# Optimization experiments

Hardware: AMD Instinct MI355X
Metric: run time of the kernel (lower is better)

Reference implementation:

```python
import jax, jax.numpy as jnp
import numpy as np

NEG = -65504.0  # torch.finfo(float16).min
EPS = 1e-6

B, T, D = 2, 1024, 2048
H, HD = 16, 128          # n_head, head_dim
K = 128                  # dynamic_w_hidden_dim
IH = 1                   # dynamic_hidden_dim = H // squeeze_ratio


def _rope(x, freqs_cis):
    # x: [B,T,H,hd]; 'half' mode: first/second half are the rotation pair,
    # output is interleaved (stack(...,-1).flatten(3) in torch).
    half = x.shape[-1] // 2
    a, b = x[..., :half], x[..., half:]
    cos = freqs_cis[None, :, None, :, 0]
    sin = freqs_cis[None, :, None, :, 1]
    out = jnp.stack([a * cos - b * sin, b * cos + a * sin], axis=-1)
    return out.reshape(x.shape)


def _cross_head_proj(inputs, qw1, qw2, kw1, kw2, qdd, kdd):
    # inputs: [B,N,T,S]; qw1/qw2: [B,T,I,N]; kw1/kw2: [B,S,I,N]; qdd: [B,T,N]; kdd: [B,S,N]
    out = inputs
    out = out + jnp.einsum('bnts,btin,btim->bmts', inputs, qw1, qw2)
    out = out + jnp.einsum('bnts,bsin,bsim->bmts', inputs, kw1, kw2)
    out = out + inputs * jnp.swapaxes(qdd, 1, 2)[..., None]   # [B,N,T,1]
    out = out + inputs * jnp.swapaxes(kdd, 1, 2)[:, :, None, :]  # [B,N,1,S]
    return out


def setup_inputs() -> dict:
    key = jax.random.key(0)
    ks = jax.random.split(key, 7)
    x = jax.random.normal(ks[0], (B, T, D), jnp.float32)
    mask = jnp.tril(jnp.ones((1, 1, T, T), bool))  # causal
    # rotary tables: [T, hd/2, 2] (cos, sin)
    inv = 1.0 / (10000.0 ** (jnp.arange(0, HD, 2, dtype=jnp.float32) / HD))
    ang = jnp.arange(T, dtype=jnp.float32)[:, None] * inv[None, :]
    freqs_cis = jnp.stack([jnp.cos(ang), jnp.sin(ang)], axis=-1)
    s = 0.02
    wqkv = jax.random.normal(ks[1], (D, 3 * H * HD), jnp.float32) * s
    wo = jax.random.normal(ks[2], (H * HD, D), jnp.float32) * s
    dw1 = jax.random.normal(ks[3], (D, 4, K), jnp.float32) * s
    qkw = jax.random.normal(ks[4], (4, K, 2 * IH, H), jnp.float32) * s
    dd_w = jax.random.normal(ks[5], (D, 4 * H), jnp.float32) * s
    return {"x": x, "mask": mask, "freqs_cis": freqs_cis, "wqkv": wqkv,
            "wo": wo, "dw1": dw1, "qkw": qkw, "dd_w": dd_w}


def reference(x, mask, freqs_cis, wqkv, wo, dw1, qkw, dd_w):
    b, t, d = x.shape
    qkv = x @ wqkv
    q, k, v = jnp.split(qkv, [H * HD, 2 * H * HD], axis=-1)
    q = q.reshape(b, t, H, HD)
    k = k.reshape(b, t, H, HD)
    v = v.reshape(b, t, H, HD)
    q = _rope(q, freqs_cis)
    k = _rope(k, freqs_cis)
    q = jnp.swapaxes(q, 1, 2) * (HD ** -0.5)  # [B,H,T,hd]
    k = jnp.swapaxes(k, 1, 2)
    v = jnp.swapaxes(v, 1, 2)

    # ---- DynamicWeightProjection (G=1, squeezed) ----
    dw_hidden = jax.nn.gelu(jnp.einsum('btd,dck->btck', x, dw1), approximate=False)
    w = jnp.einsum('btck,ckim->btcim', dw_hidden, qkw)  # [B,T,4,2*IH,H]
    w1, w2 = w[..., :IH, :], w[..., IH:, :]
    w1 = w1 * jax.lax.rsqrt(jnp.mean(w1 * w1, axis=-1, keepdims=True) + EPS)
    pre_qw1, pre_kw1, post_qw1, post_kw1 = [w1[:, :, i] for i in range(4)]
    pre_qw2, pre_kw2, post_qw2, post_kw2 = [w2[:, :, i] for i in range(4)]
    dd = jnp.tanh(x @ dd_w).reshape(b, t, 4, H)
    pre_qdd, pre_kdd, post_qdd, post_kdd = [dd[:, :, i] for i in range(4)]

    # ---- attention with cross-head mixing ----
    logits = jnp.einsum('bhtd,bhsd->bhts', q, k)
    logits = _cross_head_proj(logits, pre_qw1, pre_qw2, pre_kw1, pre_kw2, pre_qdd, pre_kdd)
    logits = jnp.where(mask, logits, NEG)
    probs = jax.nn.softmax(logits, axis=-1)
    probs = _cross_head_proj(probs, post_qw1, post_qw2, post_kw1, post_kw2, post_qdd, post_kdd)
    o = jnp.einsum('bhts,bhsd->bhtd', probs, v)
    o = jnp.swapaxes(o, 1, 2).reshape(b, t, H * HD)
    return o @ wo
```

## Files before the change

kernel.cpp:

```cpp
#include <hip/hip_runtime.h>


typedef unsigned short u16;
typedef unsigned int u32;
typedef __attribute__((ext_vector_type(8))) short s16x8;
typedef __attribute__((ext_vector_type(4))) float f32x4;
typedef __attribute__((ext_vector_type(2))) float f32x2;
typedef __attribute__((ext_vector_type(2))) u16 u16x2;
typedef __attribute__((ext_vector_type(8))) u16 u16x8;

#define DEV __device__ __forceinline__

DEV float bf2f(u16 u) { union { u32 u; float f; } a; a.u = ((u32)u) << 16; return a.f; }
DEV u16 f2bf(float f) {
  union { float f; u32 u; } a; a.f = f;
  u32 r = a.u + 0x7fffu + ((a.u >> 16) & 1u);
  return (u16)(r >> 16);
}

DEV void gload16(const void* g, void* l) {
  __builtin_amdgcn_global_load_lds((__attribute__((address_space(1))) void*)g,
                                   (__attribute__((address_space(3))) void*)l,
                                   16, 0, 0);
}

template <int OUTBF>
__global__ __launch_bounds__(256) void gemm_bt(
    const u16* __restrict__ A, const u16* __restrict__ B, void* __restrict__ Cp,
    int K, int lda, int ldb, int ldc,
    long sAb, long sBb, long sCb1, long sCb2, int CZ2, int cmode, int swz)
{
  int bx = blockIdx.x, by = blockIdx.y;
  if (swz) {
    int nx = gridDim.x;
    int fid = by * nx + bx;
    int cpx = (nx * gridDim.y) >> 3;
    int nid = (fid & 7) * cpx + (fid >> 3);
    bx = nid % nx; by = nid / nx;
  }
  if (cmode == 1 && bx > by) return;
  __shared__ u16 sA[128 * 64];
  __shared__ u16 sB[128 * 64];
  const int tid = threadIdx.x, wv = tid >> 6, ln = tid & 63;
  const int z = blockIdx.z;
  const u16* Ab = A + (size_t)z * sAb + (size_t)(by * 128) * lda;
  const u16* Bb = B + (size_t)z * sBb + (size_t)(bx * 128) * ldb;
  const int wr = (wv >> 1) * 64, wc = (wv & 1) * 64;
  const int Keff = (cmode == 2) ? min(K, (by + 1) * 128) : K;

  f32x4 acc[4][4];
#pragma unroll
  for (int m = 0; m < 4; ++m)
#pragma unroll
    for (int n = 0; n < 4; ++n) {
      f32x4 zz = {0.f, 0.f, 0.f, 0.f};
      acc[m][n] = zz;
    }

  int o_[4], r_[4], cb_[4];
#pragma unroll
  for (int i = 0; i < 4; ++i) {
    int o = (wv * 4 + i) * 1024 + ln * 16;
    o_[i] = o;
    int r = o >> 7;
    r_[i] = r;
    cb_[i] = (o & 127) ^ ((r & 7) << 4);
  }
  const int frswz = (ln & 7) << 4;
  const int fkcol = (ln >> 4) << 4;

  for (int k0 = 0; k0 < Keff; k0 += 64) {
    __syncthreads();
#pragma unroll
    for (int i = 0; i < 4; ++i)
      gload16(Ab + (size_t)r_[i] * lda + (k0 + (cb_[i] >> 1)), (char*)sA + o_[i]);
#pragma unroll
    for (int i = 0; i < 4; ++i)
      gload16(Bb + (size_t)r_[i] * ldb + (k0 + (cb_[i] >> 1)), (char*)sB + o_[i]);
    __syncthreads();

#pragma unroll
    for (int ks = 0; ks < 2; ++ks) {
      s16x8 av[4], bv[4];
#pragma unroll
      for (int m = 0; m < 4; ++m) {
        int row = wr + m * 16 + (ln & 15);
        int addr = row * 128 + ((ks * 64 + fkcol) ^ frswz);
        av[m] = *(const s16x8*)((const char*)sA + addr);
      }
#pragma unroll
      for (int n = 0; n < 4; ++n) {
        int row = wc + n * 16 + (ln & 15);
        int addr = row * 128 + ((ks * 64 + fkcol) ^ frswz);
        bv[n] = *(const s16x8*)((const char*)sB + addr);
      }
#pragma unroll
      for (int m = 0; m < 4; ++m)
#pragma unroll
        for (int n = 0; n < 4; ++n)
          acc[m][n] = __builtin_amdgcn_mfma_f32_16x16x32_bf16(av[m], bv[n], acc[m][n], 0, 0, 0);
    }
  }

  const size_t cbase = (size_t)(z / CZ2) * sCb1 + (size_t)(z % CZ2) * sCb2;
  const int r0 = by * 128 + wr + ((ln >> 4) << 2);
  const int c0 = bx * 128 + wc + (ln & 15);
#pragma unroll
  for (int m = 0; m < 4; ++m)
#pragma unroll
    for (int n = 0; n < 4; ++n)
#pragma unroll
      for (int j = 0; j < 4; ++j) {
        int row = r0 + m * 16 + j, col = c0 + n * 16;
        if (OUTBF)
          ((u16*)Cp)[cbase + (size_t)row * ldc + col] = f2bf(acc[m][n][j]);
        else
          ((float*)Cp)[cbase + (size_t)row * ldc + col] = acc[m][n][j];
      }
}

template <int INBF>
__global__ __launch_bounds__(256) void transpose_to_bf16(
    const void* __restrict__ srcv, u16* __restrict__ dst,
    int R, int C, int Cpad, int srcLd, long sSrc1, long sSrc2, int Z2, long sDst)
{
  __shared__ float tile[32][33];
  const int z = blockIdx.z, z1 = z / Z2, z2 = z % Z2;
  const size_t sbase = (size_t)z1 * sSrc1 + (size_t)z2 * sSrc2;
  u16* d = dst + (size_t)z * sDst;
  const int c0 = blockIdx.x * 32, r0 = blockIdx.y * 32;
  const int tx = threadIdx.x, ty = threadIdx.y;
#pragma unroll
  for (int i = 0; i < 4; ++i) {
    int r = r0 + ty + i * 8, c = c0 + tx;
    float v = 0.f;
    if (c < C && r < R) {
      if (INBF) v = bf2f(((const u16*)srcv)[sbase + (size_t)r * srcLd + c]);
      else      v = ((const float*)srcv)[sbase + (size_t)r * srcLd + c];
    }
    tile[ty + i * 8][tx] = v;
  }
  __syncthreads();
#pragma unroll
  for (int i = 0; i < 4; ++i) {
    int dr = c0 + ty + i * 8, dc = r0 + tx;
    if (dr < Cpad && dc < R) d[(size_t)dr * R + dc] = f2bf(tile[tx][ty + i * 8]);
  }
}

__global__ void cvt_f32_bf16_k(const float* __restrict__ src, u16* __restrict__ dst, int n4) {
  int i = blockIdx.x * 256 + threadIdx.x;
  if (i >= n4) return;
  const float4 v = ((const float4*)src)[i];
  u16* o = dst + (size_t)i * 4;
  o[0] = f2bf(v.x); o[1] = f2bf(v.y); o[2] = f2bf(v.z); o[3] = f2bf(v.w);
}

__global__ __launch_bounds__(256) void rope_k(
    const u16* __restrict__ qkvm, const float* __restrict__ fc,
    u16* __restrict__ qb, u16* __restrict__ kb)
{
  const int bt = blockIdx.x, b = bt >> 10, t = bt & 1023;
  const u16* row = qkvm + (size_t)bt * 6784;
  const float SC = 0.08838834764831845f;
#pragma unroll
  for (int it = 0; it < 4; ++it) {
    int idx = threadIdx.x + it * 256;
    int h = idx >> 6, j = idx & 63;
    float c = fc[(t * 64 + j) * 2], sn = fc[(t * 64 + j) * 2 + 1];
    float qa = bf2f(row[h * 128 + j]), qbv = bf2f(row[h * 128 + 64 + j]);
    float ka = bf2f(row[2048 + h * 128 + j]), kbv = bf2f(row[2048 + h * 128 + 64 + j]);
    size_t o = ((size_t)(b * 16 + h) * 1024 + t) * 128 + 2 * j;
    qb[o]     = f2bf((qa * c - qbv * sn) * SC);
    qb[o + 1] = f2bf((qbv * c + qa * sn) * SC);
    kb[o]     = f2bf(ka * c - kbv * sn);
    kb[o + 1] = f2bf(kbv * c + ka * sn);
  }
}

__global__ __launch_bounds__(64) void gelu_bf16_k(u16* __restrict__ qm) {
  int bt = blockIdx.x, tid = threadIdx.x;
  u16* p = qm + (size_t)bt * 6784 + 6144 + tid * 8;
  u16x8 v = *(u16x8*)p;
#pragma unroll
  for (int i = 0; i < 8; ++i) {
    float f = bf2f(v[i]);
    f = 0.5f * f * (1.f + erff(f * 0.70710678118654752f));
    v[i] = f2bf(f);
  }
  *(u16x8*)p = v;
}

__global__ __launch_bounds__(64) void wproj_k(
    const u16* __restrict__ qkvm, const float* __restrict__ qkw,
    float* __restrict__ w1a, float* __restrict__ w2a, float* __restrict__ kpT)
{
  const int bt = blockIdx.x, ln = threadIdx.x;
  const int c = ln >> 4, m = ln & 15;
  const int b = bt >> 10, t = bt & 1023;
  const u16* hp = qkvm + (size_t)bt * 6784 + 6144 + c * 128;
  const float* Wp = qkw + (size_t)c * 4096 + m;
  float w1 = 0.f, w2 = 0.f;
  for (int k = 0; k < 128; ++k) {
    float hv = bf2f(hp[k]);
    w1 += hv * Wp[k * 32];
    w2 += hv * Wp[k * 32 + 16];
  }
  float ss = w1 * w1;
  ss += __shfl_xor(ss, 1); ss += __shfl_xor(ss, 2);
  ss += __shfl_xor(ss, 4); ss += __shfl_xor(ss, 8);
  float nrm = rsqrtf(ss * (1.f / 16.f) + 1e-6f);
  float w1n = w1 * nrm;
  size_t o = (size_t)bt * 64 + c * 16 + m;
  w1a[o] = w1n;
  w2a[o] = w2;
  size_t kb = (size_t)b * 98304 + (size_t)m * 1024 + t;
  if (c == 1) { kpT[kb] = w1n; kpT[kb + 16384] = w2; }
  if (c == 3) { kpT[kb + 49152] = w1n; kpT[kb + 65536] = w2; }
}

__global__ __launch_bounds__(64) void dd_k(const u16* __restrict__ qkvm,
                                           float* __restrict__ dda, float* __restrict__ kpT) {
  int bt = blockIdx.x, ln = threadIdx.x;
  int c = ln >> 4, m = ln & 15;
  int b = bt >> 10, t = bt & 1023;
  float v = tanhf(bf2f(qkvm[(size_t)bt * 6784 + 6656 + ln]));
  dda[(size_t)bt * 64 + ln] = v;
  size_t kb = (size_t)b * 98304 + (size_t)m * 1024 + t;
  if (c == 1) kpT[kb + 32768] = v;
  if (c == 3) kpT[kb + 81920] = v;
}

__global__ __launch_bounds__(512, 2) void proj_softmax_k(
    const float* __restrict__ L, u16* __restrict__ P,
    const float* __restrict__ w1a, const float* __restrict__ w2a,
    const float* __restrict__ dda, const float* __restrict__ kparT)
{
  const int t0 = blockIdx.x * 2, b = blockIdx.y;
  const int tid = threadIdx.x, wv = tid >> 6, ln = tid & 63;
  const int s0 = tid * 2;
  const bool liveB = (s0 <= t0 + 1);

  __shared__ float qpar[2][6][16];
  __shared__ float red2[2][16][8];
  __shared__ float rzf[2][16];
  if (tid < 192) {
    int tt = (tid >= 96) ? 1 : 0, u = tid - tt * 96;
    int a = u >> 4, hh = u & 15;
    const float* sp = (a == 0 || a == 3) ? w1a : ((a == 1 || a == 4) ? w2a : dda);
    int cc = (a < 3) ? 0 : 2;
    qpar[tt][a][hh] = sp[(size_t)(b * 1024 + t0 + tt) * 64 + cc * 16 + hh];
  }
  __syncthreads();

  const float* kp = kparT + (size_t)b * 98304 + s0;
  float vA[16][2], vB[16][2];
  const size_t lbaseA = ((size_t)(b * 16) * 1024 + t0) * 1024 + s0;
  const size_t lbaseB = lbaseA + 1024;

  if (liveB) {
#pragma unroll
    for (int h = 0; h < 16; ++h) {
      f32x2 dA = *(const f32x2*)(L + lbaseA + (size_t)h * 1048576);
      f32x2 dB = *(const f32x2*)(L + lbaseB + (size_t)h * 1048576);
      vA[h][0] = dA[0]; vA[h][1] = dA[1];
      vB[h][0] = dB[0]; vB[h][1] = dB[1];
    }
    float dqA0 = 0.f, dqA1 = 0.f, dkA0 = 0.f, dkA1 = 0.f;
    float dqB0 = 0.f, dqB1 = 0.f, dkB0 = 0.f, dkB1 = 0.f;
#pragma unroll
    for (int h = 0; h < 16; ++h) {
      f32x2 k1 = *(const f32x2*)(kp + h * 1024);
      dqA0 += vA[h][0] * qpar[0][0][h]; dqA1 += vA[h][1] * qpar[0][0][h];
      dkA0 += vA[h][0] * k1[0];         dkA1 += vA[h][1] * k1[1];
      dqB0 += vB[h][0] * qpar[1][0][h]; dqB1 += vB[h][1] * qpar[1][0][h];
      dkB0 += vB[h][0] * k1[0];         dkB1 += vB[h][1] * k1[1];
    }
    const bool okA0 = (s0 <= t0), okA1 = (s0 + 1 <= t0), okB1 = (s0 + 1 <= t0 + 1);
#pragma unroll
    for (int h = 0; h < 16; ++h) {
      f32x2 k2 = *(const f32x2*)(kp + 16384 + h * 1024);
      f32x2 kd = *(const f32x2*)(kp + 32768 + h * 1024);
      float aA0 = vA[h][0] * (1.f + qpar[0][2][h] + kd[0]) + qpar[0][1][h] * dqA0 + k2[0] * dkA0;
      float aA1 = vA[h][1] * (1.f + qpar[0][2][h] + kd[1]) + qpar[0][1][h] * dqA1 + k2[1] * dkA1;
      float aB0 = vB[h][0] * (1.f + qpar[1][2][h] + kd[0]) + qpar[1][1][h] * dqB0 + k2[0] * dkB0;
      float aB1 = vB[h][1] * (1.f + qpar[1][2][h] + kd[1]) + qpar[1][1][h] * dqB1 + k2[1] * dkB1;
      vA[h][0] = okA0 ? __expf(aA0) : 0.f;
      vA[h][1] = okA1 ? __expf(aA1) : 0.f;
      vB[h][0] = __expf(aB0);
      vB[h][1] = okB1 ? __expf(aB1) : 0.f;
    }
  } else {
#pragma unroll
    for (int h = 0; h < 16; ++h) {
      vA[h][0] = 0.f; vA[h][1] = 0.f; vB[h][0] = 0.f; vB[h][1] = 0.f;
    }
  }

#pragma unroll
  for (int h = 0; h < 16; ++h) {
    float xA = vA[h][0] + vA[h][1];
    float xB = vB[h][0] + vB[h][1];
#pragma unroll
    for (int off = 32; off > 0; off >>= 1) {
      xA += __shfl_xor(xA, off);
      xB += __shfl_xor(xB, off);
    }
    if (ln == 0) { red2[0][h][wv] = xA; red2[1][h][wv] = xB; }
  }
  __syncthreads();
  if (tid < 32) {
    int tt = tid >> 4, h = tid & 15;
    rzf[tt][h] = 1.f / (((red2[tt][h][0] + red2[tt][h][1]) + (red2[tt][h][2] + red2[tt][h][3])) +
                        ((red2[tt][h][4] + red2[tt][h][5]) + (red2[tt][h][6] + red2[tt][h][7])));
  }
  __syncthreads();

  const size_t pbaseA = lbaseA, pbaseB = lbaseB;
  if (liveB) {
    float pdqA0 = 0.f, pdqA1 = 0.f, pdkA0 = 0.f, pdkA1 = 0.f;
    float pdqB0 = 0.f, pdqB1 = 0.f, pdkB0 = 0.f, pdkB1 = 0.f;
#pragma unroll
    for (int h = 0; h < 16; ++h) {
      f32x2 k1 = *(const f32x2*)(kp + 49152 + h * 1024);
      float rzA = rzf[0][h], rzB = rzf[1][h];
      float pA0 = vA[h][0] * rzA, pA1 = vA[h][1] * rzA;
      float pB0 = vB[h][0] * rzB, pB1 = vB[h][1] * rzB;
      vA[h][0] = pA0; vA[h][1] = pA1; vB[h][0] = pB0; vB[h][1] = pB1;
      pdqA0 += pA0 * qpar[0][3][h]; pdqA1 += pA1 * qpar[0][3][h];
      pdkA0 += pA0 * k1[0];         pdkA1 += pA1 * k1[1];
      pdqB0 += pB0 * qpar[1][3][h]; pdqB1 += pB1 * qpar[1][3][h];
      pdkB0 += pB0 * k1[0];         pdkB1 += pB1 * k1[1];
    }
#pragma unroll
    for (int h = 0; h < 16; ++h) {
      f32x2 k2 = *(const f32x2*)(kp + 65536 + h * 1024);
      f32x2 kd = *(const f32x2*)(kp + 81920 + h * 1024);
      u16x2 pkA, pkB;
      pkA[0] = f2bf(vA[h][0] * (1.f + qpar[0][5][h] + kd[0]) + qpar[0][4][h] * pdqA0 + k2[0] * pdkA0);
      pkA[1] = f2bf(vA[h][1] * (1.f + qpar[0][5][h] + kd[1]) + qpar[0][4][h] * pdqA1 + k2[1] * pdkA1);
      pkB[0] = f2bf(vB[h][0] * (1.f + qpar[1][5][h] + kd[0]) + qpar[1][4][h] * pdqB0 + k2[0] * pdkB0);
      pkB[1] = f2bf(vB[h][1] * (1.f + qpar[1][5][h] + kd[1]) + qpar[1][4][h] * pdqB1 + k2[1] * pdkB1);
      *(u16x2*)(P + pbaseA + (size_t)h * 1048576) = pkA;
      *(u16x2*)(P + pbaseB + (size_t)h * 1048576) = pkB;
    }
  } else {
    u16x2 z2 = {0, 0};
#pragma unroll
    for (int h = 0; h < 16; ++h) {
      *(u16x2*)(P + pbaseA + (size_t)h * 1048576) = z2;
      *(u16x2*)(P + pbaseB + (size_t)h * 1048576) = z2;
    }
  }
}

extern "C" void kernel_launch(void* const* d_in, const int* in_sizes, int n_in,
                              void* d_out, int out_size, void* d_ws, size_t ws_size,
                              hipStream_t stream)
{
  (void)in_sizes; (void)n_in; (void)out_size; (void)ws_size;
  const float* x    = (const float*)d_in[0];
  const float* fc   = (const float*)d_in[2];
  const float* wqkv = (const float*)d_in[3];
  const float* wo   = (const float*)d_in[4];
  const float* dw1  = (const float*)d_in[5];
  const float* qkw  = (const float*)d_in[6];
  const float* ddw  = (const float*)d_in[7];
  float* out = (float*)d_out;
  char* w = (char*)d_ws;

  u16*   woT   = (u16*)(w + 0);
  u16*   qb    = (u16*)(w + 8388608);
  u16*   kb    = (u16*)(w + 16777216);
  u16*   vT    = (u16*)(w + 25165824);
  u16*   obf   = (u16*)(w + 33554432);
  float* w1a   = (float*)(w + 41943040);
  float* w2a   = (float*)(w + 42467328);
  float* dda   = (float*)(w + 42991616);
  const size_t TB = 43515904;
  u16*   xb    = (u16*)(w + TB);
  u16*   wallT = (u16*)(w + TB + 8388608);
  u16*   qkvm  = (u16*)(w + TB + 36175872);
  float* L     = (float*)(w + TB);
  u16*   P     = (u16*)(w + TB + 134217728);
  float* kparT = (float*)(w + 244842496);

  cvt_f32_bf16_k<<<4096, 256, 0, stream>>>(x, xb, 1048576);
  transpose_to_bf16<0><<<dim3(192, 64, 1), dim3(32, 8), 0, stream>>>(wqkv, wallT, 2048, 6144, 6144, 6144, 0, 0, 1, 0);
  transpose_to_bf16<0><<<dim3(16, 64, 1),  dim3(32, 8), 0, stream>>>(dw1,  wallT + (size_t)6144 * 2048, 2048, 512, 512, 512, 0, 0, 1, 0);
  transpose_to_bf16<0><<<dim3(4, 64, 1),   dim3(32, 8), 0, stream>>>(ddw,  wallT + (size_t)6656 * 2048, 2048, 64, 128, 64, 0, 0, 1, 0);
  transpose_to_bf16<0><<<dim3(64, 64, 1),  dim3(32, 8), 0, stream>>>(wo,   woT, 2048, 2048, 2048, 2048, 0, 0, 1, 0);

  gemm_bt<1><<<dim3(53, 16, 1), 256, 0, stream>>>(xb, wallT, qkvm, 2048, 2048, 2048, 6784, 0, 0, 0, 0, 1, 0, 1);
  rope_k<<<2048, 256, 0, stream>>>(qkvm, fc, qb, kb);
  transpose_to_bf16<1><<<dim3(4, 32, 32), dim3(32, 8), 0, stream>>>(qkvm + 4096, vT, 1024, 128, 128, 6784, 6946816, 128, 16, 131072);

  gelu_bf16_k<<<2048, 64, 0, stream>>>(qkvm);
  wproj_k<<<2048, 64, 0, stream>>>(qkvm, qkw, w1a, w2a, kparT);
  dd_k<<<2048, 64, 0, stream>>>(qkvm, dda, kparT);

  gemm_bt<0><<<dim3(8, 8, 32), 256, 0, stream>>>(qb, kb, L, 128, 128, 128, 1024, 131072, 131072, 1048576, 0, 1, 1, 0);
  proj_softmax_k<<<dim3(512, 2, 1), 512, 0, stream>>>(L, P, w1a, w2a, dda, kparT);
  gemm_bt<1><<<dim3(1, 8, 32), 256, 0, stream>>>(P, vT, obf, 1024, 1024, 1024, 2048, 1048576, 131072, 2097152, 128, 16, 2, 0);

  gemm_bt<0><<<dim3(16, 16, 1), 256, 0, stream>>>(obf, woT, out, 2048, 2048, 2048, 2048, 0, 0, 0, 0, 1, 0, 1);
}
```

Measured before the change: 325.1 us.

## Use 256x256 double-buffered MFMA GEMM for fused QKV/gating projection

```diff
diff --git a/kernel.cpp b/kernel.cpp
--- a/kernel.cpp
+++ b/kernel.cpp
@@ -22,6 +22,118 @@
   __builtin_amdgcn_global_load_lds((__attribute__((address_space(1))) void*)g,
                                    (__attribute__((address_space(3))) void*)l,
                                    16, 0, 0);
+}
+
+template <int OUTBF>
+__global__ __launch_bounds__(512, 1) void gemm256(
+    const u16* __restrict__ A, const u16* __restrict__ B, void* __restrict__ Cp,
+    int K, int lda, int ldb, int ldc)
+{
+  __shared__ u16 sA[2][256 * 64];
+  __shared__ u16 sB[2][256 * 64];
+  const int tid = threadIdx.x, ln = tid & 63;
+  const int wid = tid >> 6, wm = wid >> 2, wn = wid & 3;
+
+  const int nx = gridDim.x;
+  const int fid = blockIdx.y * nx + blockIdx.x;
+  const int cpx = (nx * gridDim.y) >> 3;
+  const int nid = (fid & 7) * cpx + (fid >> 3);
+  const int bx = nid % nx, by = nid / nx;
+
+  const u16* Ab = A + (size_t)(by * 256) * lda;
+  const u16* Bb = B + (size_t)(bx * 256) * ldb;
+
+  f32x4 acc[8][4];
+#pragma unroll
+  for (int m = 0; m < 8; ++m)
+#pragma unroll
+    for (int n = 0; n < 4; ++n) {
+      f32x4 zz = {0.f, 0.f, 0.f, 0.f};
+      acc[m][n] = zz;
+    }
+
+  int srow[4], scol[4], soff[4];
+#pragma unroll
+  for (int i = 0; i < 4; ++i) {
+    int o = i * 8192 + tid * 16;
+    soff[i] = o;
+    srow[i] = o >> 7;
+    scol[i] = (o & 127) >> 1;
+  }
+
+#define STAGE256(ba, bb, k0)                                              \
+  {                                                                       \
+    _Pragma("unroll")                                                     \
+    for (int i_ = 0; i_ < 4; ++i_)                                        \
+      gload16(Ab + (size_t)srow[i_] * lda + (k0) + scol[i_],              \
+              (char*)(ba) + soff[i_]);                                    \
+    _Pragma("unroll")                                                     \
+    for (int i_ = 0; i_ < 4; ++i_)                                        \
+      gload16(Bb + (size_t)srow[i_] * ldb + (k0) + scol[i_],              \
+              (char*)(bb) + soff[i_]);                                    \
+  }
+
+  const int arow = wm * 128 + (ln & 15);
+  const int brow = wn * 64 + (ln & 15);
+  const int kb = (ln >> 4) * 16;
+  const int NT = K >> 6;
+
+  STAGE256(sA[0], sB[0], 0);
+  asm volatile("s_waitcnt vmcnt(0)" ::: "memory");
+  __builtin_amdgcn_s_barrier();
+
+  for (int t = 0; t < NT; ++t) {
+    const int c = t & 1;
+    const char* pa = (const char*)sA[c];
+    const char* pb = (const char*)sB[c];
+    s16x8 bfr[4][2];
+#pragma unroll
+    for (int ph = 0; ph < 4; ++ph) {
+      if (ph == 0) {
+        if (t + 1 < NT) STAGE256(sA[c ^ 1], sB[c ^ 1], (t + 1) * 64);
+#pragma unroll
+        for (int n = 0; n < 4; ++n)
+#pragma unroll
+          for (int kk = 0; kk < 2; ++kk)
+            bfr[n][kk] = *(const s16x8*)(pb + (size_t)(brow + n * 16) * 128 + kk * 64 + kb);
+      }
+      s16x8 afr[2][2];
+#pragma unroll
+      for (int mm = 0; mm < 2; ++mm)
+#pragma unroll
+        for (int kk = 0; kk < 2; ++kk)
+          afr[mm][kk] = *(const s16x8*)(pa + (size_t)(arow + (ph * 2 + mm) * 16) * 128 + kk * 64 + kb);
+      __builtin_amdgcn_s_barrier();
+      __builtin_amdgcn_s_setprio(1);
+#pragma unroll
+      for (int mm = 0; mm < 2; ++mm)
+#pragma unroll
+        for (int n = 0; n < 4; ++n)
+#pragma unroll
+          for (int kk = 0; kk < 2; ++kk)
+            acc[ph * 2 + mm][n] = __builtin_amdgcn_mfma_f32_16x16x32_bf16(
+                afr[mm][kk], bfr[n][kk], acc[ph * 2 + mm][n], 0, 0, 0);
+      __builtin_amdgcn_s_setprio(0);
+    }
+    asm volatile("s_waitcnt vmcnt(0)" ::: "memory");
+    __builtin_amdgcn_s_barrier();
+  }
+#undef STAGE256
+
+  const int r0 = by * 256 + wm * 128 + ((ln >> 4) << 2);
+  const int c0 = bx * 256 + wn * 64 + (ln & 15);
+#pragma unroll
+  for (int m = 0; m < 8; ++m)
+#pragma unroll
+    for (int n = 0; n < 4; ++n)
+#pragma unroll
+      for (int j = 0; j < 4; ++j) {
+        int row = r0 + m * 16 + j, col = c0 + n * 16;
+        if (OUTBF)
+          ((u16*)Cp)[(size_t)row * ldc + col] = f2bf(acc[m][n][j]);
+        else
+          ((float*)Cp)[(size_t)row * ldc + col] = acc[m][n][j];
+      }
 }
 
 template <int OUTBF>
@@ -161,7 +273,7 @@
     u16* __restrict__ qb, u16* __restrict__ kb)
 {
   const int bt = blockIdx.x, b = bt >> 10, t = bt & 1023;
-  const u16* row = qkvm + (size_t)bt * 6784;
+  const u16* row = qkvm + (size_t)bt * 6912;
   const float SC = 0.08838834764831845f;
 #pragma unroll
   for (int it = 0; it < 4; ++it) {
@@ -180,7 +292,7 @@
 
 __global__ __launch_bounds__(64) void gelu_bf16_k(u16* __restrict__ qm) {
   int bt = blockIdx.x, tid = threadIdx.x;
-  u16* p = qm + (size_t)bt * 6784 + 6144 + tid * 8;
+  u16* p = qm + (size_t)bt * 6912 + 6144 + tid * 8;
   u16x8 v = *(u16x8*)p;
 #pragma unroll
   for (int i = 0; i < 8; ++i) {
@@ -198,7 +310,7 @@
   const int bt = blockIdx.x, ln = threadIdx.x;
   const int c = ln >> 4, m = ln & 15;
   const int b = bt >> 10, t = bt & 1023;
-  const u16* hp = qkvm + (size_t)bt * 6784 + 6144 + c * 128;
+  const u16* hp = qkvm + (size_t)bt * 6912 + 6144 + c * 128;
   const float* Wp = qkw + (size_t)c * 4096 + m;
   float w1 = 0.f, w2 = 0.f;
   for (int k = 0; k < 128; ++k) {
@@ -224,7 +336,7 @@
   int bt = blockIdx.x, ln = threadIdx.x;
   int c = ln >> 4, m = ln & 15;
   int b = bt >> 10, t = bt & 1023;
-  float v = tanhf(bf2f(qkvm[(size_t)bt * 6784 + 6656 + ln]));
+  float v = tanhf(bf2f(qkvm[(size_t)bt * 6912 + 6656 + ln]));
   dda[(size_t)bt * 64 + ln] = v;
   size_t kb = (size_t)b * 98304 + (size_t)m * 1024 + t;
   if (c == 1) kpT[kb + 32768] = v;
@@ -380,7 +492,7 @@
   const size_t TB = 43515904;
   u16*   xb    = (u16*)(w + TB);
   u16*   wallT = (u16*)(w + TB + 8388608);
-  u16*   qkvm  = (u16*)(w + TB + 36175872);
+  u16*   qkvm  = (u16*)(w + TB + 36700160);
   float* L     = (float*)(w + TB);
   u16*   P     = (u16*)(w + TB + 134217728);
   float* kparT = (float*)(w + 244842496);
@@ -388,12 +500,12 @@
   cvt_f32_bf16_k<<<4096, 256, 0, stream>>>(x, xb, 1048576);
   transpose_to_bf16<0><<<dim3(192, 64, 1), dim3(32, 8), 0, stream>>>(wqkv, wallT, 2048, 6144, 6144, 6144, 0, 0, 1, 0);
   transpose_to_bf16<0><<<dim3(16, 64, 1),  dim3(32, 8), 0, stream>>>(dw1,  wallT + (size_t)6144 * 2048, 2048, 512, 512, 512, 0, 0, 1, 0);
-  transpose_to_bf16<0><<<dim3(4, 64, 1),   dim3(32, 8), 0, stream>>>(ddw,  wallT + (size_t)6656 * 2048, 2048, 64, 128, 64, 0, 0, 1, 0);
+  transpose_to_bf16<0><<<dim3(8, 64, 1),   dim3(32, 8), 0, stream>>>(ddw,  wallT + (size_t)6656 * 2048, 2048, 64, 256, 64, 0, 0, 1, 0);
   transpose_to_bf16<0><<<dim3(64, 64, 1),  dim3(32, 8), 0, stream>>>(wo,   woT, 2048, 2048, 2048, 2048, 0, 0, 1, 0);
 
-  gemm_bt<1><<<dim3(53, 16, 1), 256, 0, stream>>>(xb, wallT, qkvm, 2048, 2048, 2048, 6784, 0, 0, 0, 0, 1, 0, 1);
+  gemm256<1><<<dim3(27, 8, 1), 512, 0, stream>>>(xb, wallT, qkvm, 2048, 2048, 2048, 6912);
   rope_k<<<2048, 256, 0, stream>>>(qkvm, fc, qb, kb);
-  transpose_to_bf16<1><<<dim3(4, 32, 32), dim3(32, 8), 0, stream>>>(qkvm + 4096, vT, 1024, 128, 128, 6784, 6946816, 128, 16, 131072);
+  transpose_to_bf16<1><<<dim3(4, 32, 32), dim3(32, 8), 0, stream>>>(qkvm + 4096, vT, 1024, 128, 128, 6912, 7077888, 128, 16, 131072);
 
   gelu_bf16_k<<<2048, 64, 0, stream>>>(qkvm);
   wproj_k<<<2048, 64, 0, stream>>>(qkvm, qkw, w1a, w2a, kparT);
```

After: 322.9 us. About the same (-0.7%).
